# Optimization experiments

Hardware: AMD Instinct MI355X
Metric: run time of the kernel (lower is better)

The kernel has to match this reference:

```python
import jax, jax.numpy as jnp
import numpy as np

H = 4
N = 50000
D_IN = 128
D_MODEL = 256
NCLASS = 40
B_S = 1
BH = B_S * H
LN_EPS = 1e-5


def sparse_perm_1D(indices, values, feats, n, bh):
    """Batched sparse (bh,n,n) @ dense (bh,n,d): gather -> scale -> segment-sum scatter."""
    gathered = feats[indices[0], indices[2]]              # (nnz, d)
    contrib = values[:, None] * gathered                   # (nnz, d)
    seg = indices[0] * n + indices[1]                      # (nnz,)
    out = jax.ops.segment_sum(contrib, seg, num_segments=bh * n)
    return out.reshape(bh, n, -1)


def layer_norm(x, gamma, beta):
    mu = jnp.mean(x, axis=-1, keepdims=True)
    var = jnp.var(x, axis=-1, keepdims=True)
    return (x - mu) * jax.lax.rsqrt(var + LN_EPS) * gamma + beta


def setup_inputs() -> dict:
    key = jax.random.key(0)
    k1, k2, k3, k4, k5, k6, k7 = jax.random.split(key, 7)
    # per-(batch*head) permutation sigma: nonzero at (b, i, sigma_b(i))
    perm_keys = jax.random.split(k1, BH)
    sigma = jax.vmap(lambda k: jax.random.permutation(k, N))(perm_keys)  # (BH, N)
    b_idx = jnp.repeat(jnp.arange(BH), N)
    row_idx = jnp.tile(jnp.arange(N), BH)
    col_idx = sigma.reshape(-1)
    perm_indices = jnp.stack([b_idx, row_idx, col_idx], axis=0).astype(jnp.int32)  # (3, BH*N)
    perm_values = jax.random.uniform(k2, (BH * N,), dtype=jnp.float32)
    features = jax.random.normal(k3, (B_S, N, D_IN), dtype=jnp.float32)
    appd = jax.random.normal(k4, (B_S, N, D_IN), dtype=jnp.float32)
    # parameters
    w_scale_in = 1.0 / np.sqrt(2 * D_IN)
    W_in = jax.random.uniform(k5, (2 * D_IN, D_MODEL), dtype=jnp.float32, minval=-w_scale_in, maxval=w_scale_in)
    b_in = jnp.zeros((D_MODEL,), dtype=jnp.float32)
    ln_gamma = jnp.ones((D_MODEL * H,), dtype=jnp.float32)
    ln_beta = jnp.zeros((D_MODEL * H,), dtype=jnp.float32)
    w_scale_h = 1.0 / np.sqrt(D_MODEL * H)
    W_head = jax.random.uniform(k6, (D_MODEL * H, NCLASS), dtype=jnp.float32, minval=-w_scale_h, maxval=w_scale_h)
    b_head = jax.random.uniform(k7, (NCLASS,), dtype=jnp.float32, minval=-w_scale_h, maxval=w_scale_h)
    return {"perm_indices": perm_indices, "perm_values": perm_values,
            "features": features, "appd": appd,
            "W_in": W_in, "b_in": b_in,
            "ln_gamma": ln_gamma, "ln_beta": ln_beta,
            "W_head": W_head, "b_head": b_head}


def reference(perm_indices, perm_values, features, appd, W_in, b_in, ln_gamma, ln_beta, W_head, b_head):
    # concat auxiliary features, replicate per head: (B_S,N,2*D_IN) -> (BH,N,2*D_IN)
    feat = jnp.concatenate([features, appd], axis=-1)
    feat = jnp.broadcast_to(feat[:, None], (B_S, H, N, 2 * D_IN)).reshape(BH, N, 2 * D_IN)
    # permute rows: perm @ feat
    x = sparse_perm_1D(perm_indices, perm_values, feat, N, BH)
    # ff_in + relu (dropout is identity at eval)
    x = jax.nn.relu(x @ W_in + b_in)                       # (BH, N, D_MODEL)
    # nlayers == nblocks == 0: compress/uncompress loops are empty
    # inverse permutation: perm^T @ x (swap row/col indices)
    idx_t = jnp.stack([perm_indices[0], perm_indices[2], perm_indices[1]], axis=0)
    y = sparse_perm_1D(idx_t, perm_values, x, N, BH)       # (BH, N, D_MODEL)
    # (B_S,H,N,D) -> (B_S,N,H*D)
    y = y.reshape(B_S, H, N, D_MODEL).transpose(0, 2, 1, 3).reshape(B_S, N, H * D_MODEL)
    y = layer_norm(y, ln_gamma, ln_beta)
    return y @ W_head + b_head                             # (B_S, N, NCLASS)
```

## Files before the change

kernel.cpp:

```cpp
#include <hip/hip_runtime.h>
#include <hip/hip_bf16.h>

#define NROW 50000
#define DIN 128
#define DM 256
#define HH 4
#define NC 40
#define BHN 200000
#define NBLK 1563

typedef float f32x4 __attribute__((ext_vector_type(4)));
typedef short bf16x8 __attribute__((ext_vector_type(8)));

__device__ __forceinline__ unsigned short f2bf(float x) {
    unsigned int u = __float_as_uint(x);
    u += 0x7fffu + ((u >> 16) & 1u);
    return (unsigned short)(u >> 16);
}

__device__ __forceinline__ unsigned int pk2(float lo, float hi) {
    __hip_bfloat162 h = __float22bfloat162_rn(make_float2(lo, hi));
    return *(unsigned int*)&h;
}

__device__ __forceinline__ float bf2f(unsigned short s) {
    return __uint_as_float(((unsigned int)s) << 16);
}

__global__ __launch_bounds__(256) void k_prep(const int* __restrict__ pi,
                                              const float* __restrict__ pv,
                                              const float* __restrict__ Win,
                                              const float* __restrict__ Wh,
                                              const float* __restrict__ gamma,
                                              const float* __restrict__ beta,
                                              const float* __restrict__ bh,
                                              float* __restrict__ vcol,
                                              unsigned short* __restrict__ Wpk,
                                              unsigned short* __restrict__ Wgpk,
                                              float* __restrict__ bias2,
                                              float* __restrict__ cs) {
    const int bid = blockIdx.x, tid = threadIdx.x;
    if (bid < 782) {
        int k = bid * 256 + tid;
        if (k < BHN) {
            int b = (k >= 150000) ? 3 : (k >= 100000) ? 2 : (k >= 50000) ? 1 : 0;
            int col = pi[2 * BHN + k];
            vcol[b * NROW + col] = pv[k];
        }
    } else if (bid < 798) {
        int base = (bid - 782) * 512;
        #pragma unroll
        for (int q = 0; q < 2; ++q) {
            int s = base + q * 256 + tid;
            int ln = s & 63;
            int t  = (s >> 6) & 15;
            int kc = s >> 10;
            int n  = t * 16 + (ln & 15);
            int kb = kc * 32 + ((ln >> 4) << 3);
            union { unsigned int ui[4]; uint4 v4; } u;
            #pragma unroll
            for (int jj = 0; jj < 4; ++jj)
                u.ui[jj] = pk2(Win[(kb + 2 * jj) * DM + n], Win[(kb + 2 * jj + 1) * DM + n]);
            *(uint4*)&Wpk[s * 8] = u.v4;
        }
    } else if (bid < 810) {
        int base = (bid - 798) * 512;
        #pragma unroll
        for (int q = 0; q < 2; ++q) {
            int s = base + q * 256 + tid;
            int ln = s & 63;
            int u6 = s >> 6;
            int t  = u6 % 3;
            int v6 = u6 / 3;
            int kc = v6 & 7;
            int h  = v6 >> 3;
            int c  = t * 16 + (ln & 15);
            int d0 = h * 256 + kc * 32 + ((ln >> 4) << 3);
            union { unsigned int ui[4]; uint4 v4; } u;
            if (c < NC) {
                #pragma unroll
                for (int jj = 0; jj < 4; ++jj)
                    u.ui[jj] = pk2(gamma[d0 + 2 * jj] * Wh[(d0 + 2 * jj) * NC + c],
                                   gamma[d0 + 2 * jj + 1] * Wh[(d0 + 2 * jj + 1) * NC + c]);
            } else {
                u.v4 = make_uint4(0u, 0u, 0u, 0u);
            }
            *(uint4*)&Wgpk[s * 8] = u.v4;
        }
    } else {
        __shared__ float red[256], red2[256];
        int c = bid - 810;
        float sb = 0.f, sc = 0.f;
        #pragma unroll
        for (int q = 0; q < 4; ++q) {
            int d = tid + 256 * q;
            float w = Wh[d * NC + c];
            sb = fmaf(beta[d], w, sb);
            sc = fmaf(gamma[d], w, sc);
        }
        red[tid] = sb; red2[tid] = sc;
        __syncthreads();
        for (int st = 128; st > 0; st >>= 1) {
            if (tid < st) { red[tid] += red[tid + st]; red2[tid] += red2[tid + st]; }
            __syncthreads();
        }
        if (tid == 0) { bias2[c] = bh[c] + red[0]; cs[c] = red2[0]; }
    }
}

__global__ __launch_bounds__(64, 2) void k_fused(
    const float* __restrict__ feats, const float* __restrict__ appd,
    const unsigned short* __restrict__ Wpk,
    const unsigned short* __restrict__ Wgpk,
    const float* __restrict__ vcol,
    const float* __restrict__ b_in,
    const float* __restrict__ bias2,
    const float* __restrict__ cs,
    float* __restrict__ out)
{
    __shared__ __align__(16) unsigned short Gb[32 * 264];
    __shared__ float rsS[32], rmS[32];

    const int tid = threadIdx.x;
    const int quad = tid >> 4;
    const int lr = tid & 15;
    const int j0 = blockIdx.x * 32;

    const int ar0 = min(j0 + lr, NROW - 1);
    const int ar1 = min(j0 + 16 + lr, NROW - 1);

    float vhh[2][HH][4];
    #pragma unroll
    for (int rt = 0; rt < 2; ++rt)
        #pragma unroll
        for (int h = 0; h < HH; ++h)
            #pragma unroll
            for (int rg = 0; rg < 4; ++rg)
                vhh[rt][h][rg] = vcol[h * NROW + min(j0 + rt * 16 + quad * 4 + rg, NROW - 1)];

    const f32x4 zero4 = {0.f, 0.f, 0.f, 0.f};
    float s_[2][4] = {}, ss_[2][4] = {};

    #pragma unroll
    for (int ch = 0; ch < 2; ++ch) {
        f32x4 accG[2][8];
        #pragma unroll
        for (int rt = 0; rt < 2; ++rt)
            #pragma unroll
            for (int t = 0; t < 8; ++t) accG[rt][t] = zero4;

        #pragma unroll
        for (int kc = 0; kc < 8; ++kc) {
            const float* src = (kc < 4) ? feats : appd;
            const int ko = (kc & 3) * 32 + quad * 8;
            union { unsigned int ui[4]; bf16x8 v; } a0, a1;
            {
                float4 x0 = *(const float4*)&src[(size_t)ar0 * DIN + ko];
                float4 x1 = *(const float4*)&src[(size_t)ar0 * DIN + ko + 4];
                a0.ui[0] = pk2(x0.x, x0.y); a0.ui[1] = pk2(x0.z, x0.w);
                a0.ui[2] = pk2(x1.x, x1.y); a0.ui[3] = pk2(x1.z, x1.w);
                float4 y0 = *(const float4*)&src[(size_t)ar1 * DIN + ko];
                float4 y1 = *(const float4*)&src[(size_t)ar1 * DIN + ko + 4];
                a1.ui[0] = pk2(y0.x, y0.y); a1.ui[1] = pk2(y0.z, y0.w);
                a1.ui[2] = pk2(y1.x, y1.y); a1.ui[3] = pk2(y1.z, y1.w);
            }
            #pragma unroll
            for (int t = 0; t < 8; ++t) {
                bf16x8 bf = *(const bf16x8*)&Wpk[(size_t)(((kc * 16 + ch * 8 + t) << 6) + tid) * 8];
                accG[0][t] = __builtin_amdgcn_mfma_f32_16x16x32_bf16(a0.v, bf, accG[0][t], 0, 0, 0);
                accG[1][t] = __builtin_amdgcn_mfma_f32_16x16x32_bf16(a1.v, bf, accG[1][t], 0, 0, 0);
            }
        }
        float bt[8];
        #pragma unroll
        for (int t = 0; t < 8; ++t) bt[t] = b_in[(ch * 8 + t) * 16 + lr];
        #pragma unroll
        for (int rt = 0; rt < 2; ++rt)
            #pragma unroll
            for (int t = 0; t < 8; ++t)
                #pragma unroll
                for (int rg = 0; rg < 4; ++rg) {
                    float gg = accG[rt][t][rg];
                    Gb[(rt * 16 + quad * 4 + rg) * 264 + (ch * 8 + t) * 16 + lr] = f2bf(gg);
                    #pragma unroll
                    for (int h = 0; h < HH; ++h) {
                        float v = vhh[rt][h][rg];
                        float y = v * fmaxf(fmaf(v, gg, bt[t]), 0.f);
                        s_[rt][rg] += y;
                        ss_[rt][rg] = fmaf(y, y, ss_[rt][rg]);
                    }
                }
    }

    #pragma unroll
    for (int m = 1; m <= 8; m <<= 1)
        #pragma unroll
        for (int rt = 0; rt < 2; ++rt)
            #pragma unroll
            for (int rg = 0; rg < 4; ++rg) {
                s_[rt][rg] += __shfl_xor(s_[rt][rg], m);
                ss_[rt][rg] += __shfl_xor(ss_[rt][rg], m);
            }
    if (lr == 0) {
        #pragma unroll
        for (int rt = 0; rt < 2; ++rt)
            #pragma unroll
            for (int rg = 0; rg < 4; ++rg) {
                float mm = s_[rt][rg] * (1.f / 1024.f);
                float var = ss_[rt][rg] * (1.f / 1024.f) - mm * mm;
                float r_ = rsqrtf(var + 1e-5f);
                rsS[rt * 16 + quad * 4 + rg] = r_;
                rmS[rt * 16 + quad * 4 + rg] = r_ * mm;
            }
    }
    __syncthreads();

    float vm[HH][2];
    #pragma unroll
    for (int h = 0; h < HH; ++h) {
        vm[h][0] = vcol[h * NROW + min(j0 + lr, NROW - 1)];
        vm[h][1] = vcol[h * NROW + min(j0 + 16 + lr, NROW - 1)];
    }

    f32x4 accO[HH][2][3];
    #pragma unroll
    for (int h = 0; h < HH; ++h)
        #pragma unroll
        for (int rt = 0; rt < 2; ++rt)
            #pragma unroll
            for (int t = 0; t < 3; ++t) accO[h][rt][t] = zero4;

    #pragma unroll
    for (int kc = 0; kc < 8; ++kc) {
        bf16x8 gf0 = *(const bf16x8*)&Gb[lr * 264 + kc * 32 + quad * 8];
        bf16x8 gf1 = *(const bf16x8*)&Gb[(16 + lr) * 264 + kc * 32 + quad * 8];
        float4 bA = *(const float4*)&b_in[kc * 32 + quad * 8];
        float4 bB = *(const float4*)&b_in[kc * 32 + quad * 8 + 4];
        float bb[8] = {bA.x, bA.y, bA.z, bA.w, bB.x, bB.y, bB.z, bB.w};
        float g0[8], g1[8];
        #pragma unroll
        for (int j = 0; j < 8; ++j) {
            g0[j] = bf2f((unsigned short)gf0[j]);
            g1[j] = bf2f((unsigned short)gf1[j]);
        }
        #pragma unroll
        for (int h = 0; h < HH; ++h) {
            union { unsigned int ui[4]; bf16x8 v; } u0, u1;
            #pragma unroll
            for (int jj = 0; jj < 4; ++jj) {
                float ya = fmaxf(fmaf(vm[h][0], g0[2 * jj], bb[2 * jj]), 0.f);
                float yb = fmaxf(fmaf(vm[h][0], g0[2 * jj + 1], bb[2 * jj + 1]), 0.f);
                u0.ui[jj] = pk2(ya, yb);
                float yc = fmaxf(fmaf(vm[h][1], g1[2 * jj], bb[2 * jj]), 0.f);
                float yd = fmaxf(fmaf(vm[h][1], g1[2 * jj + 1], bb[2 * jj + 1]), 0.f);
                u1.ui[jj] = pk2(yc, yd);
            }
            #pragma unroll
            for (int t = 0; t < 3; ++t) {
                bf16x8 wf = *(const bf16x8*)&Wgpk[(size_t)((((h * 8 + kc) * 3 + t) << 6) + tid) * 8];
                accO[h][0][t] = __builtin_amdgcn_mfma_f32_16x16x32_bf16(u0.v, wf, accO[h][0][t], 0, 0, 0);
                accO[h][1][t] = __builtin_amdgcn_mfma_f32_16x16x32_bf16(u1.v, wf, accO[h][1][t], 0, 0, 0);
            }
        }
    }

    float ct[3], b2[3];
    #pragma unroll
    for (int t = 0; t < 3; ++t) {
        int c = t * 16 + lr;
        ct[t] = (c < NC) ? cs[c] : 0.f;
        b2[t] = (c < NC) ? bias2[c] : 0.f;
    }
    #pragma unroll
    for (int rt = 0; rt < 2; ++rt)
        #pragma unroll
        for (int rg = 0; rg < 4; ++rg) {
            int rr = rt * 16 + quad * 4 + rg;
            int row = j0 + rr;
            if (row < NROW) {
                float rsv = rsS[rr], rmv = rmS[rr];
                #pragma unroll
                for (int t = 0; t < 3; ++t) {
                    int c = t * 16 + lr;
                    if (c < NC) {
                        float raw = vhh[rt][0][rg] * accO[0][rt][t][rg];
                        raw = fmaf(vhh[rt][1][rg], accO[1][rt][t][rg], raw);
                        raw = fmaf(vhh[rt][2][rg], accO[2][rt][t][rg], raw);
                        raw = fmaf(vhh[rt][3][rg], accO[3][rt][t][rg], raw);
                        float base = fmaf(-rmv, ct[t], b2[t]);
                        out[(size_t)row * NC + c] = fmaf(rsv, raw, base);
                    }
                }
            }
        }
}

extern "C" void kernel_launch(void* const* d_in, const int* in_sizes, int n_in,
                              void* d_out, int out_size, void* d_ws, size_t ws_size,
                              hipStream_t stream) {
    const int*   pi    = (const int*)d_in[0];
    const float* pv    = (const float*)d_in[1];
    const float* feats = (const float*)d_in[2];
    const float* appd  = (const float*)d_in[3];
    const float* Win   = (const float*)d_in[4];
    const float* b_in  = (const float*)d_in[5];
    const float* gamma = (const float*)d_in[6];
    const float* beta  = (const float*)d_in[7];
    const float* Wh    = (const float*)d_in[8];
    const float* bh    = (const float*)d_in[9];
    float* out = (float*)d_out;

    char* w = (char*)d_ws;
    float*          vcolW  = (float*)w;
    unsigned short* WpkW   = (unsigned short*)(w + 800000);
    unsigned short* WgpkW  = (unsigned short*)(w + 931072);
    float*          bias2W = (float*)(w + 1029376);
    float*          csW    = (float*)(w + 1029536);

    k_prep<<<850, 256, 0, stream>>>(pi, pv, Win, Wh, gamma, beta, bh, vcolW, WpkW, WgpkW, bias2W, csW);
    k_fused<<<NBLK, 64, 0, stream>>>(feats, appd, WpkW, WgpkW, vcolW, b_in, bias2W, csW, out);
}
```

Measured before the change: 158.2 us.

## Halve rows per block to 16 and fold head accumulation to cut registers

New measurement: 191.9 us. +21.3%, slower.

```diff
diff --git a/kernel.cpp b/kernel.cpp
--- a/kernel.cpp
+++ b/kernel.cpp
@@ -7,7 +7,7 @@
 #define HH 4
 #define NC 40
 #define BHN 200000
-#define NBLK 1563
+#define NBLK 3125
 
 typedef float f32x4 __attribute__((ext_vector_type(4)));
 typedef short bf16x8 __attribute__((ext_vector_type(8)));
@@ -108,7 +108,7 @@
     }
 }
 
-__global__ __launch_bounds__(64, 2) void k_fused(
+__global__ __launch_bounds__(64, 3) void k_fused(
     const float* __restrict__ feats, const float* __restrict__ appd,
     const unsigned short* __restrict__ Wpk,
     const unsigned short* __restrict__ Wgpk,
@@ -118,181 +118,130 @@
     const float* __restrict__ cs,
     float* __restrict__ out)
 {
-    __shared__ __align__(16) unsigned short Gb[32 * 264];
-    __shared__ float rsS[32], rmS[32];
+    __shared__ __align__(16) unsigned short Gb[16 * 264];
+    __shared__ float rsS[16], rmS[16];
 
     const int tid = threadIdx.x;
     const int quad = tid >> 4;
     const int lr = tid & 15;
-    const int j0 = blockIdx.x * 32;
-
-    const int ar0 = min(j0 + lr, NROW - 1);
-    const int ar1 = min(j0 + 16 + lr, NROW - 1);
-
-    float vhh[2][HH][4];
-    #pragma unroll
-    for (int rt = 0; rt < 2; ++rt)
-        #pragma unroll
-        for (int h = 0; h < HH; ++h)
-            #pragma unroll
-            for (int rg = 0; rg < 4; ++rg)
-                vhh[rt][h][rg] = vcol[h * NROW + min(j0 + rt * 16 + quad * 4 + rg, NROW - 1)];
+    const int j0 = blockIdx.x * 16;
+    const int ar = j0 + lr;
 
     const f32x4 zero4 = {0.f, 0.f, 0.f, 0.f};
-    float s_[2][4] = {}, ss_[2][4] = {};
-
-    #pragma unroll
-    for (int ch = 0; ch < 2; ++ch) {
-        f32x4 accG[2][8];
-        #pragma unroll
-        for (int rt = 0; rt < 2; ++rt)
-            #pragma unroll
-            for (int t = 0; t < 8; ++t) accG[rt][t] = zero4;
-
+
+    f32x4 accG[16];
+    #pragma unroll
+    for (int t = 0; t < 16; ++t) accG[t] = zero4;
+
+    #pragma unroll
+    for (int kc = 0; kc < 8; ++kc) {
+        const float* src = (kc < 4) ? feats : appd;
+        const int ko = (kc & 3) * 32 + quad * 8;
+        float4 x0 = *(const float4*)&src[(size_t)ar * DIN + ko];
+        float4 x1 = *(const float4*)&src[(size_t)ar * DIN + ko + 4];
+        union { unsigned int ui[4]; bf16x8 v; } a;
+        a.ui[0] = pk2(x0.x, x0.y); a.ui[1] = pk2(x0.z, x0.w);
+        a.ui[2] = pk2(x1.x, x1.y); a.ui[3] = pk2(x1.z, x1.w);
+        #pragma unroll
+        for (int t = 0; t < 16; ++t) {
+            bf16x8 bf = *(const bf16x8*)&Wpk[(size_t)(((kc * 16 + t) << 6) + tid) * 8];
+            accG[t] = __builtin_amdgcn_mfma_f32_16x16x32_bf16(a.v, bf, accG[t], 0, 0, 0);
+        }
+    }
+
+    float vhh[HH][4];
+    #pragma unroll
+    for (int h = 0; h < HH; ++h)
+        #pragma unroll
+        for (int rg = 0; rg < 4; ++rg)
+            vhh[h][rg] = vcol[h * NROW + j0 + quad * 4 + rg];
+
+    float s_[4] = {0.f, 0.f, 0.f, 0.f}, ss_[4] = {0.f, 0.f, 0.f, 0.f};
+    #pragma unroll
+    for (int t = 0; t < 16; ++t) {
+        float bt = b_in[t * 16 + lr];
+        #pragma unroll
+        for (int rg = 0; rg < 4; ++rg) {
+            float gg = accG[t][rg];
+            Gb[(quad * 4 + rg) * 264 + t * 16 + lr] = f2bf(gg);
+            #pragma unroll
+            for (int h = 0; h < HH; ++h) {
+                float v = vhh[h][rg];
+                float y = v * fmaxf(fmaf(v, gg, bt), 0.f);
+                s_[rg] += y;
+                ss_[rg] = fmaf(y, y, ss_[rg]);
+            }
+        }
+    }
+    #pragma unroll
+    for (int m = 1; m <= 8; m <<= 1)
+        #pragma unroll
+        for (int rg = 0; rg < 4; ++rg) {
+            s_[rg] += __shfl_xor(s_[rg], m);
+            ss_[rg] += __shfl_xor(ss_[rg], m);
+        }
+    if (lr == 0) {
+        #pragma unroll
+        for (int rg = 0; rg < 4; ++rg) {
+            float mm = s_[rg] * (1.f / 1024.f);
+            float var = ss_[rg] * (1.f / 1024.f) - mm * mm;
+            float r_ = rsqrtf(var + 1e-5f);
+            rsS[quad * 4 + rg] = r_;
+            rmS[quad * 4 + rg] = r_ * mm;
+        }
+    }
+    __syncthreads();
+
+    f32x4 accT[3];
+    #pragma unroll
+    for (int t = 0; t < 3; ++t) accT[t] = zero4;
+
+    #pragma unroll
+    for (int h = 0; h < HH; ++h) {
+        const float vmh = vcol[h * NROW + ar];
+        f32x4 accP[3];
+        #pragma unroll
+        for (int t = 0; t < 3; ++t) accP[t] = zero4;
         #pragma unroll
         for (int kc = 0; kc < 8; ++kc) {
-            const float* src = (kc < 4) ? feats : appd;
-            const int ko = (kc & 3) * 32 + quad * 8;
-            union { unsigned int ui[4]; bf16x8 v; } a0, a1;
-            {
-                float4 x0 = *(const float4*)&src[(size_t)ar0 * DIN + ko];
-                float4 x1 = *(const float4*)&src[(size_t)ar0 * DIN + ko + 4];
-                a0.ui[0] = pk2(x0.x, x0.y); a0.ui[1] = pk2(x0.z, x0.w);
-                a0.ui[2] = pk2(x1.x, x1.y); a0.ui[3] = pk2(x1.z, x1.w);
-                float4 y0 = *(const float4*)&src[(size_t)ar1 * DIN + ko];
-                float4 y1 = *(const float4*)&src[(size_t)ar1 * DIN + ko + 4];
-                a1.ui[0] = pk2(y0.x, y0.y); a1.ui[1] = pk2(y0.z, y0.w);
-                a1.ui[2] = pk2(y1.x, y1.y); a1.ui[3] = pk2(y1.z, y1.w);
-            }
-            #pragma unroll
-            for (int t = 0; t < 8; ++t) {
-                bf16x8 bf = *(const bf16x8*)&Wpk[(size_t)(((kc * 16 + ch * 8 + t) << 6) + tid) * 8];
-                accG[0][t] = __builtin_amdgcn_mfma_f32_16x16x32_bf16(a0.v, bf, accG[0][t], 0, 0, 0);
-                accG[1][t] = __builtin_amdgcn_mfma_f32_16x16x32_bf16(a1.v, bf, accG[1][t], 0, 0, 0);
-            }
-        }
-        float bt[8];
-        #pragma unroll
-        for (int t = 0; t < 8; ++t) bt[t] = b_in[(ch * 8 + t) * 16 + lr];
-        #pragma unroll
-        for (int rt = 0; rt < 2; ++rt)
-            #pragma unroll
-            for (int t = 0; t < 8; ++t)
-                #pragma unroll
-                for (int rg = 0; rg < 4; ++rg) {
-                    float gg = accG[rt][t][rg];
-                    Gb[(rt * 16 + quad * 4 + rg) * 264 + (ch * 8 + t) * 16 + lr] = f2bf(gg);
-                    #pragma unroll
-                    for (int h = 0; h < HH; ++h) {
-                        float v = vhh[rt][h][rg];
-                        float y = v * fmaxf(fmaf(v, gg, bt[t]), 0.f);
-                        s_[rt][rg] += y;
-                        ss_[rt][rg] = fmaf(y, y, ss_[rt][rg]);
-                    }
-                }
-    }
-
-    #pragma unroll
-    for (int m = 1; m <= 8; m <<= 1)
-        #pragma unroll
-        for (int rt = 0; rt < 2; ++rt)
-            #pragma unroll
-            for (int rg = 0; rg < 4; ++rg) {
-                s_[rt][rg] += __shfl_xor(s_[rt][rg], m);
-                ss_[rt][rg] += __shfl_xor(ss_[rt][rg], m);
-            }
-    if (lr == 0) {
-        #pragma unroll
-        for (int rt = 0; rt < 2; ++rt)
-            #pragma unroll
-            for (int rg = 0; rg < 4; ++rg) {
-                float mm = s_[rt][rg] * (1.f / 1024.f);
-                float var = ss_[rt][rg] * (1.f / 1024.f) - mm * mm;
-                float r_ = rsqrtf(var + 1e-5f);
-                rsS[rt * 16 + quad * 4 + rg] = r_;
-                rmS[rt * 16 + quad * 4 + rg] = r_ * mm;
-            }
-    }
-    __syncthreads();
-
-    float vm[HH][2];
-    #pragma unroll
-    for (int h = 0; h < HH; ++h) {
-        vm[h][0] = vcol[h * NROW + min(j0 + lr, NROW - 1)];
-        vm[h][1] = vcol[h * NROW + min(j0 + 16 + lr, NROW - 1)];
-    }
-
-    f32x4 accO[HH][2][3];
-    #pragma unroll
-    for (int h = 0; h < HH; ++h)
-        #pragma unroll
-        for (int rt = 0; rt < 2; ++rt)
-            #pragma unroll
-            for (int t = 0; t < 3; ++t) accO[h][rt][t] = zero4;
-
-    #pragma unroll
-    for (int kc = 0; kc < 8; ++kc) {
-        bf16x8 gf0 = *(const bf16x8*)&Gb[lr * 264 + kc * 32 + quad * 8];
-        bf16x8 gf1 = *(const bf16x8*)&Gb[(16 + lr) * 264 + kc * 32 + quad * 8];
-        float4 bA = *(const float4*)&b_in[kc * 32 + quad * 8];
-        float4 bB = *(const float4*)&b_in[kc * 32 + quad * 8 + 4];
-        float bb[8] = {bA.x, bA.y, bA.z, bA.w, bB.x, bB.y, bB.z, bB.w};
-        float g0[8], g1[8];
-        #pragma unroll
-        for (int j = 0; j < 8; ++j) {
-            g0[j] = bf2f((unsigned short)gf0[j]);
-            g1[j] = bf2f((unsigned short)gf1[j]);
-        }
-        #pragma unroll
-        for (int h = 0; h < HH; ++h) {
-            union { unsigned int ui[4]; bf16x8 v; } u0, u1;
+            bf16x8 gf = *(const bf16x8*)&Gb[lr * 264 + kc * 32 + quad * 8];
+            float4 bA = *(const float4*)&b_in[kc * 32 + quad * 8];
+            float4 bB = *(const float4*)&b_in[kc * 32 + quad * 8 + 4];
+            float bb[8] = {bA.x, bA.y, bA.z, bA.w, bB.x, bB.y, bB.z, bB.w};
+            union { unsigned int ui[4]; bf16x8 v; } u;
             #pragma unroll
             for (int jj = 0; jj < 4; ++jj) {
-                float ya = fmaxf(fmaf(vm[h][0], g0[2 * jj], bb[2 * jj]), 0.f);
-                float yb = fmaxf(fmaf(vm[h][0], g0[2 * jj + 1], bb[2 * jj + 1]), 0.f);
-                u0.ui[jj] = pk2(ya, yb);
-                float yc = fmaxf(fmaf(vm[h][1], g1[2 * jj], bb[2 * jj]), 0.f);
-                float yd = fmaxf(fmaf(vm[h][1], g1[2 * jj + 1], bb[2 * jj + 1]), 0.f);
-                u1.ui[jj] = pk2(yc, yd);
+                float ya = fmaxf(fmaf(vmh, bf2f((unsigned short)gf[2 * jj]), bb[2 * jj]), 0.f);
+                float yb = fmaxf(fmaf(vmh, bf2f((unsigned short)gf[2 * jj + 1]), bb[2 * jj + 1]), 0.f);
+                u.ui[jj] = pk2(ya, yb);
             }
             #pragma unroll
             for (int t = 0; t < 3; ++t) {
                 bf16x8 wf = *(const bf16x8*)&Wgpk[(size_t)((((h * 8 + kc) * 3 + t) << 6) + tid) * 8];
-                accO[h][0][t] = __builtin_amdgcn_mfma_f32_16x16x32_bf16(u0.v, wf, accO[h][0][t], 0, 0, 0);
-                accO[h][1][t] = __builtin_amdgcn_mfma_f32_16x16x32_bf16(u1.v, wf, accO[h][1][t], 0, 0, 0);
-            }
-        }
-    }
-
-    float ct[3], b2[3];
+                accP[t] = __builtin_amdgcn_mfma_f32_16x16x32_bf16(u.v, wf, accP[t], 0, 0, 0);
+            }
+        }
+        #pragma unroll
+        for (int t = 0; t < 3; ++t)
+            #pragma unroll
+            for (int rg = 0; rg < 4; ++rg)
+                accT[t][rg] = fmaf(vhh[h][rg], accP[t][rg], accT[t][rg]);
+    }
+
     #pragma unroll
     for (int t = 0; t < 3; ++t) {
         int c = t * 16 + lr;
-        ct[t] = (c < NC) ? cs[c] : 0.f;
-        b2[t] = (c < NC) ? bias2[c] : 0.f;
-    }
-    #pragma unroll
-    for (int rt = 0; rt < 2; ++rt)
-        #pragma unroll
-        for (int rg = 0; rg < 4; ++rg) {
-            int rr = rt * 16 + quad * 4 + rg;
-            int row = j0 + rr;
-            if (row < NROW) {
-                float rsv = rsS[rr], rmv = rmS[rr];
-                #pragma unroll
-                for (int t = 0; t < 3; ++t) {
-                    int c = t * 16 + lr;
-                    if (c < NC) {
-                        float raw = vhh[rt][0][rg] * accO[0][rt][t][rg];
-                        raw = fmaf(vhh[rt][1][rg], accO[1][rt][t][rg], raw);
-                        raw = fmaf(vhh[rt][2][rg], accO[2][rt][t][rg], raw);
-                        raw = fmaf(vhh[rt][3][rg], accO[3][rt][t][rg], raw);
-                        float base = fmaf(-rmv, ct[t], b2[t]);
-                        out[(size_t)row * NC + c] = fmaf(rsv, raw, base);
-                    }
-                }
-            }
-        }
+        if (c < NC) {
+            float ct = cs[c];
+            float b2 = bias2[c];
+            #pragma unroll
+            for (int rg = 0; rg < 4; ++rg) {
+                int rr = quad * 4 + rg;
+                float base = fmaf(-rmS[rr], ct, b2);
+                out[(size_t)(j0 + rr) * NC + c] = fmaf(rsS[rr], accT[t][rg], base);
+            }
+        }
+    }
 }
 
 extern "C" void kernel_launch(void* const* d_in, const int* in_sizes, int n_in,
```
